# Optimization experiments

Hardware: AMD Instinct MI355X
Metric: run time of the kernel (lower is better)

## Reference

```python
import jax, jax.numpy as jnp
import numpy as np

N = 100000      # nodes
E = 3200000     # edges
F_IN = 78       # num_features_mol
F_GAT = 256     # mol_out_feats
HEADS = 2
F_HYP = 128     # mol_out_feats_hyper


def setup_inputs() -> dict:
    key = jax.random.key(0)
    ks = jax.random.split(key, 32)
    g = lambda k, s: jax.random.normal(k, s, dtype=jnp.float32) * 0.05
    inp = {}
    inp["mol_x"] = jax.random.normal(ks[0], (N, F_IN), dtype=jnp.float32)
    inp["mol_edge_index"] = jax.random.randint(ks[1], (2, E), 0, N)
    inp["hyper_edge"] = jax.random.randint(ks[2], (2, E), 0, N)
    # GAT layer 1 (78 -> 256, 2 heads, concat=False)
    inp["W1"] = g(ks[3], (F_IN, HEADS * F_GAT)); inp["as1"] = g(ks[4], (HEADS, F_GAT)); inp["ad1"] = g(ks[5], (HEADS, F_GAT)); inp["b1"] = jnp.zeros((F_GAT,), jnp.float32)
    # GAT layers 2,3 (256 -> 256)
    inp["W2"] = g(ks[6], (F_GAT, HEADS * F_GAT)); inp["as2"] = g(ks[7], (HEADS, F_GAT)); inp["ad2"] = g(ks[8], (HEADS, F_GAT)); inp["b2"] = jnp.zeros((F_GAT,), jnp.float32)
    inp["W3"] = g(ks[9], (F_GAT, HEADS * F_GAT)); inp["as3"] = g(ks[10], (HEADS, F_GAT)); inp["ad3"] = g(ks[11], (HEADS, F_GAT)); inp["b3"] = jnp.zeros((F_GAT,), jnp.float32)
    # GRU-style gating fusion
    inp["fc1_w"] = g(ks[12], (F_GAT, F_GAT)); inp["fc1_b"] = jnp.zeros((F_GAT,), jnp.float32)
    inp["fc2_w"] = g(ks[13], (F_GAT, F_GAT)); inp["fc2_b"] = jnp.zeros((F_GAT,), jnp.float32)
    inp["mol_bias"] = jax.random.uniform(ks[14], (1, F_GAT), jnp.float32, -0.2, 0.2)
    # HypergraphConv layers (334 -> 128 -> 128)
    inp["theta1"] = g(ks[15], (F_GAT + F_IN, F_HYP)); inp["hb1"] = jnp.zeros((F_HYP,), jnp.float32)
    inp["theta2"] = g(ks[16], (F_HYP, F_HYP)); inp["hb2"] = jnp.zeros((F_HYP,), jnp.float32)
    return inp


def _gat(x, src, dst, W, a_s, a_d, b):
    # PyG GATConv, heads=2, concat=False, eval mode (no dropout), self-loops pre-added in src/dst
    xh = (x @ W).reshape(N, HEADS, F_GAT)            # [N,H,C]
    a_src = (xh * a_s).sum(-1)                        # [N,H]
    a_dst = (xh * a_d).sum(-1)                        # [N,H]
    e = jax.nn.leaky_relu(a_src[src] + a_dst[dst], 0.2)  # [E',H]
    m = jax.ops.segment_max(e, dst, num_segments=N)
    ex = jnp.exp(e - m[dst])
    s = jax.ops.segment_sum(ex, dst, num_segments=N)
    alpha = ex / s[dst]                               # softmax over incoming edges
    out = jax.ops.segment_sum(xh[src] * alpha[:, :, None], dst, num_segments=N)
    return out.mean(axis=1) + b                       # concat=False -> head mean


def _hyper(x, node, edge, theta, b):
    # PyG HypergraphConv, use_attention=False: D^-1 H B^-1 H^T X Theta + b
    xt = x @ theta
    ones = jnp.ones((node.shape[0],), xt.dtype)
    D = jax.ops.segment_sum(ones, node, num_segments=N)
    B = jax.ops.segment_sum(ones, edge, num_segments=N)
    Dinv = jnp.where(D > 0, 1.0 / D, 0.0)
    Binv = jnp.where(B > 0, 1.0 / B, 0.0)
    ef = Binv[:, None] * jax.ops.segment_sum(xt[node], edge, num_segments=N)
    nf = Dinv[:, None] * jax.ops.segment_sum(ef[edge], node, num_segments=N)
    return nf + b


def _forward(mol_x, mol_edge_index, hyper_edge,
             W1, as1, ad1, b1, W2, as2, ad2, b2, W3, as3, ad3, b3,
             fc1_w, fc1_b, fc2_w, fc2_b, mol_bias, theta1, hb1, theta2, hb2):
    loops = jnp.arange(N, dtype=mol_edge_index.dtype)
    src = jnp.concatenate([mol_edge_index[0], loops])
    dst = jnp.concatenate([mol_edge_index[1], loops])
    hyper_x0 = jax.lax.stop_gradient(mol_x)  # .clone().detach()
    # layer 0
    h = jax.nn.relu(_gat(mol_x, src, dst, W1, as1, ad1, b1))
    # layer 1 (relu) + gate
    x = jax.nn.relu(_gat(h, src, dst, W2, as2, ad2, b2))
    z = jax.nn.sigmoid(x @ fc1_w.T + fc1_b + h @ fc2_w.T + fc2_b + mol_bias)
    h = z * x + (1.0 - z) * h
    # layer 2 (no relu) + gate
    x = _gat(h, src, dst, W3, as3, ad3, b3)
    z = jax.nn.sigmoid(x @ fc1_w.T + fc1_b + h @ fc2_w.T + fc2_b + mol_bias)
    h = z * x + (1.0 - z) * h
    # hypergraph branch (source uses mol_edge_index here, hyper_edge is unused)
    hx = jnp.concatenate([jax.lax.stop_gradient(h), hyper_x0], axis=1)
    node, edge = mol_edge_index[0], mol_edge_index[1]
    hx = jax.nn.relu(_hyper(hx, node, edge, theta1, hb1))
    hx = jax.nn.relu(_hyper(hx, node, edge, theta2, hb2))
    return jnp.concatenate([h, hx], axis=1)  # [N, 384]


def reference(mol_x, mol_edge_index, hyper_edge,
              W1, as1, ad1, b1, W2, as2, ad2, b2, W3, as3, ad3, b3,
              fc1_w, fc1_b, fc2_w, fc2_b, mol_bias, theta1, hb1, theta2, hb2):
    return _forward(mol_x, mol_edge_index, hyper_edge,
                    W1, as1, ad1, b1, W2, as2, ad2, b2, W3, as3, ad3, b3,
                    fc1_w, fc1_b, fc2_w, fc2_b, mol_bias, theta1, hb1, theta2, hb2)
```

## Files before the change

kernel.cpp:

```cpp
#include <hip/hip_runtime.h>

typedef unsigned short u16;
typedef __attribute__((ext_vector_type(8))) short short8v;
typedef __attribute__((ext_vector_type(8))) unsigned short ushort8v;
typedef __attribute__((ext_vector_type(4))) unsigned short ushort4v;
typedef __attribute__((ext_vector_type(4))) float f32x4;
typedef __attribute__((ext_vector_type(2))) float f32x2;

__device__ __forceinline__ float bf2f(u16 u) {
    union { unsigned int i; float f; } v; v.i = ((unsigned int)u) << 16; return v.f;
}
__device__ __forceinline__ u16 f2bf(float f) {
    union { float f; unsigned int i; } v; v.f = f;
    unsigned int i = v.i;
    return (u16)((i + 0x7FFFu + ((i >> 16) & 1u)) >> 16);
}
__device__ __forceinline__ float leaky02(float x) { return x > 0.f ? x : 0.2f * x; }
__device__ __forceinline__ float load_in(const void* p, long i, int isbf) {
    return isbf ? bf2f(((const u16*)p)[i]) : ((const float*)p)[i];
}
__device__ __forceinline__ f32x2 pk_fma(f32x2 a, f32x2 b, f32x2 c) {
    f32x2 d;
    asm("v_pk_fma_f32 %0, %1, %2, %3" : "=v"(d) : "v"(a), "v"(b), "v"(c));
    return d;
}
__device__ __forceinline__ f32x2 pk_add(f32x2 a, f32x2 b) {
    f32x2 d;
    asm("v_pk_add_f32 %0, %1, %2" : "=v"(d) : "v"(a), "v"(b));
    return d;
}
__device__ __forceinline__ f32x2 bfpair(unsigned int d) {
    union { unsigned int i; float f; } lo, hi;
    lo.i = d << 16;
    hi.i = d & 0xFFFF0000u;
    f32x2 r; r.x = lo.f; r.y = hi.f; return r;
}
__device__ __forceinline__ float bperm_f(int addr, float v) {
    return __int_as_float(__builtin_amdgcn_ds_bpermute(addr, __float_as_int(v)));
}
__device__ __forceinline__ int bperm_i(int addr, int v) {
    return __builtin_amdgcn_ds_bpermute(addr, v);
}
#define GLD_LDS16(g, s) __builtin_amdgcn_global_load_lds( \
    (const __attribute__((address_space(1))) void*)(g),   \
    (__attribute__((address_space(3))) void*)(s), 16, 0, 0)

__global__ void detect_kernel(const unsigned* __restrict__ w, int* __restrict__ flag) {
    __shared__ int cnt;
    int t = threadIdx.x;
    if (t == 0) cnt = 0;
    __syncthreads();
    unsigned x = w[t * 16];
    unsigned lo = x & 0xFFFFu;
    int e = (int)((x >> 7) & 0xFFu);
    int good = (lo == 0u) || (e >= 100 && e <= 140);
    atomicAdd(&cnt, good);
    __syncthreads();
    if (t == 0) *flag = (cnt > 128) ? 1 : 0;
}

#define CSR_NBK 1024

__global__ __launch_bounds__(256)
void bucket_count_kernel(const int* __restrict__ ei, int* __restrict__ bcs,
                         int* __restrict__ bcd, int E_, int n, int SH) {
    __shared__ int hs[CSR_NBK], hd[CSR_NBK];
    const int t = threadIdx.x;
    for (int i = t; i < CSR_NBK; i += 256) { hs[i] = 0; hd[i] = 0; }
    __syncthreads();
    const int e0 = blockIdx.x * 4096;
    #pragma unroll
    for (int k = 0; k < 16; ++k) {
        int e = e0 + k * 256 + t;
        if (e < E_) {
            int s = ei[e], d = ei[E_ + e];
            if ((unsigned)s >= (unsigned)n) s = 0;
            if ((unsigned)d >= (unsigned)n) d = 0;
            atomicAdd(&hs[s >> SH], 1);
            atomicAdd(&hd[d >> SH], 1);
        }
    }
    __syncthreads();
    for (int i = t; i < CSR_NBK; i += 256) {
        if (hs[i]) atomicAdd(&bcs[i], hs[i]);
        if (hd[i]) atomicAdd(&bcd[i], hd[i]);
    }
}

__global__ void scan_excl_kernel(const int* __restrict__ deg, int* __restrict__ ptr, int n) {
    __shared__ int s_woff[17];
    __shared__ int s_carry;
    const int t = threadIdx.x;
    const int lane = t & 63, wid = t >> 6;
    if (t == 0) s_carry = 0;
    __syncthreads();
    for (int base = 0; base < n; base += 1024) {
        int i = base + t;
        int v = (i < n) ? deg[i] : 0;
        int incl = v;
        #pragma unroll
        for (int d = 1; d < 64; d <<= 1) {
            int x = __shfl_up(incl, d, 64);
            if (lane >= d) incl += x;
        }
        if (lane == 63) s_woff[wid] = incl;
        __syncthreads();
        if (t == 0) {
            int run = 0;
            #pragma unroll
            for (int w = 0; w < 16; ++w) { int x = s_woff[w]; s_woff[w] = run; run += x; }
            s_woff[16] = run;
        }
        __syncthreads();
        int excl = s_carry + s_woff[wid] + incl - v;
        if (i < n) ptr[i] = excl;
        __syncthreads();
        if (t == 0) s_carry += s_woff[16];
        __syncthreads();
    }
    if (t == 0) ptr[n] = s_carry;
}

__global__ void copy2_kernel(const int* __restrict__ a, int* __restrict__ b,
                             const int* __restrict__ c, int* __restrict__ d2, int n) {
    int i = blockIdx.x * 256 + threadIdx.x;
    if (i < n) { b[i] = a[i]; d2[i] = c[i]; }
}

__global__ __launch_bounds__(256)
void partition_kernel(const int* __restrict__ ei, int* __restrict__ bcur_s,
                      int* __restrict__ bcur_d, int2* __restrict__ ps,
                      int2* __restrict__ pd, int E_, int n, int SH) {
    __shared__ int cs[CSR_NBK], cd[CSR_NBK], bs[CSR_NBK], bd[CSR_NBK];
    const int t = threadIdx.x;
    for (int i = t; i < CSR_NBK; i += 256) { cs[i] = 0; cd[i] = 0; }
    __syncthreads();
    const int e0 = blockIdx.x * 4096;
    int sv[16], dv[16];
    #pragma unroll
    for (int k = 0; k < 16; ++k) {
        int e = e0 + k * 256 + t;
        int s = -1, d = 0;
        if (e < E_) {
            s = ei[e]; d = ei[E_ + e];
            if ((unsigned)s >= (unsigned)n) s = 0;
            if ((unsigned)d >= (unsigned)n) d = 0;
            atomicAdd(&cs[s >> SH], 1);
            atomicAdd(&cd[d >> SH], 1);
        }
        sv[k] = (e < E_) ? s : -1;
        dv[k] = d;
    }
    __syncthreads();
    for (int i = t; i < CSR_NBK; i += 256) {
        bs[i] = cs[i] ? atomicAdd(&bcur_s[i], cs[i]) : 0;
        bd[i] = cd[i] ? atomicAdd(&bcur_d[i], cd[i]) : 0;
        cs[i] = 0; cd[i] = 0;
    }
    __syncthreads();
    #pragma unroll
    for (int k = 0; k < 16; ++k) {
        int s = sv[k];
        if (s < 0) continue;
        int d = dv[k];
        int p = bs[s >> SH] + atomicAdd(&cs[s >> SH], 1);
        ps[p] = make_int2(d, s);
        int q = bd[d >> SH] + atomicAdd(&cd[d >> SH], 1);
        pd[q] = make_int2(s, d);
    }
}

__global__ __launch_bounds__(256)
void fill_bucket_kernel(const int2* __restrict__ pairs, const int* __restrict__ bptr,
                        int* __restrict__ ptr, int* __restrict__ idx, int n, int SH) {
    __shared__ int cnt[256];
    __shared__ int wsum[5];
    const int b = blockIdx.x;
    const int n0 = b << SH;
    if (n0 >= n) return;
    const int nn = min(1 << SH, n - n0);
    const int t = threadIdx.x;
    cnt[t] = 0;
    __syncthreads();
    const int pbeg = bptr[b], pend = bptr[b + 1];
    for (int j = pbeg + t; j < pend; j += 256)
        atomicAdd(&cnt[pairs[j].y - n0], 1);
    __syncthreads();
    const int c = (t < nn) ? cnt[t] : 0;
    int v = c;
    const int lane = t & 63, wid = t >> 6;
    #pragma unroll
    for (int d = 1; d < 64; d <<= 1) {
        int x = __shfl_up(v, d, 64);
        if (lane >= d) v += x;
    }
    if (lane == 63) wsum[wid] = v;
    __syncthreads();
    if (t == 0) {
        int r = 0;
        #pragma unroll
        for (int w = 0; w < 4; ++w) { int x = wsum[w]; wsum[w] = r; r += x; }
        wsum[4] = r;
    }
    __syncthreads();
    v += wsum[wid];
    const int excl = pbeg + v - c;
    __syncthreads();
    if (t < nn) { cnt[t] = excl; ptr[n0 + t] = excl; }
    if (t == 0 && n0 + nn == n) ptr[n] = pbeg + wsum[4];
    __syncthreads();
    for (int j = pbeg + t; j < pend; j += 256) {
        int2 pr = pairs[j];
        int p = atomicAdd(&cnt[pr.y - n0], 1);
        idx[p] = pr.x;
    }
}

__global__ void ingest_transpose_kernel(const void* __restrict__ src, long base,
                                        u16* __restrict__ dst, int K, int Nc, int Kp,
                                        const int* __restrict__ flag) {
    int i = blockIdx.x * 256 + threadIdx.x;
    if (i >= Nc * Kp) return;
    int n = i / Kp, k = i - n * Kp;
    float v = (k < K) ? load_in(src, base + (long)k * Nc + n, *flag) : 0.f;
    dst[i] = f2bf(v);
}

__global__ void ingest_vecs_kernel(const void* __restrict__ s0, const void* __restrict__ s1,
                                   const void* __restrict__ s2, const void* __restrict__ s3,
                                   const void* __restrict__ s4, const void* __restrict__ s5,
                                   const void* __restrict__ s6, const void* __restrict__ s7,
                                   u16* __restrict__ d0, u16* __restrict__ d1,
                                   u16* __restrict__ d2, u16* __restrict__ d3,
                                   u16* __restrict__ d4, u16* __restrict__ d5,
                                   u16* __restrict__ d6, u16* __restrict__ d7,
                                   const int* __restrict__ flag) {
    const void* srcs[8] = {s0, s1, s2, s3, s4, s5, s6, s7};
    u16* dsts[8] = {d0, d1, d2, d3, d4, d5, d6, d7};
    const int b = blockIdx.x, t = threadIdx.x;
    const int nsz = (b < 6) ? 256 : 128;
    if (t < nsz) dsts[b][t] = f2bf(load_in(srcs[b], t, *flag));
}

__global__ void ingest_wcat_kernel(const void* __restrict__ W, u16* __restrict__ dst,
                                   int Kin, int Fh, const int* __restrict__ flag) {
    int i = blockIdx.x * 256 + threadIdx.x;
    int tot = 256 * 2 * Fh;
    if (i >= tot) return;
    int o = i / (2 * Fh), k = i - o * 2 * Fh;
    int h = k / Fh, c = k - h * Fh;
    float v = (c < Kin) ? 0.5f * load_in(W, (long)c * 512 + h * 256 + o, *flag) : 0.f;
    dst[i] = f2bf(v);
}

__global__ void ingest_bcat_kernel(const void* __restrict__ fc1, const void* __restrict__ fc2,
                                   u16* __restrict__ dst, const int* __restrict__ flag) {
    int i = blockIdx.x * 256 + threadIdx.x;
    if (i >= 256 * 512) return;
    int o = i >> 9, k = i & 511;
    float v = (k < 256) ? load_in(fc1, (long)o * 256 + k, *flag)
                        : load_in(fc2, (long)o * 256 + k - 256, *flag);
    dst[i] = f2bf(v);
}

__global__ void ingest_pad_molx_kernel(const void* __restrict__ x, u16* __restrict__ dst,
                                       int ldd, int total, const int* __restrict__ flag) {
    int i = blockIdx.x * 256 + threadIdx.x;
    if (i >= total) return;
    int r = i / 96, c = i - r * 96;
    float v = (c < 78) ? load_in(x, (long)r * 78 + c, *flag) : 0.f;
    dst[(size_t)r * ldd + c] = f2bf(v);
}

__global__ void attn_vec_kernel(const void* __restrict__ W, const void* __restrict__ as_,
                                const void* __restrict__ ad_, float* __restrict__ was,
                                float* __restrict__ wad, int Kin, int Fh,
                                const int* __restrict__ flag) {
    int i = blockIdx.x * 256 + threadIdx.x;
    if (i >= 2 * Fh) return;
    int h = i / Fh, c = i - h * Fh;
    float s = 0.f, d = 0.f;
    if (c < Kin) {
        int f = *flag;
        for (int o = 0; o < 256; ++o) {
            float w = load_in(W, (long)c * 512 + h * 256 + o, f);
            s += w * load_in(as_, h * 256 + o, f);
            d += w * load_in(ad_, h * 256 + o, f);
        }
    }
    was[i] = s; wad[i] = d;
}

__global__ __launch_bounds__(256, 2)
void gemm_kernel(const u16* __restrict__ A, int lda,
                 const u16* __restrict__ Bt, int ldb,
                 u16* __restrict__ C, int ldc, int K, int M, int beta,
                 const u16* __restrict__ bias, int relu) {
    __shared__ __align__(16) u16 As[128 * 32];
    __shared__ __align__(16) u16 Bs[128 * 32];
    const int tid = threadIdx.x;
    const int wave = tid >> 6, lane = tid & 63;
    const int m0 = blockIdx.x * 128;
    const int n0 = blockIdx.y * 128;
    const int wm = (wave & 1) * 64, wn = (wave >> 1) * 64;
    const int r = lane & 15, q = lane >> 4;

    f32x4 acc[4][4];
    if (beta) {
        #pragma unroll
        for (int i = 0; i < 4; ++i)
            #pragma unroll
            for (int j = 0; j < 4; ++j)
                #pragma unroll
                for (int rr = 0; rr < 4; ++rr) {
                    size_t gr = (size_t)(m0 + wm + 16 * i + q * 4 + rr);
                    int gc = n0 + wn + 16 * j + r;
                    acc[i][j][rr] = bf2f(C[gr * ldc + gc]);
                }
    } else {
        #pragma unroll
        for (int i = 0; i < 4; ++i)
            #pragma unroll
            for (int j = 0; j < 4; ++j) acc[i][j] = (f32x4)0.f;
    }

    const int rowT = wave * 16 + (lane >> 2);
    const int koff = (lane & 3) * 8;
    int rA0 = m0 + rowT;       if (rA0 > M - 1) rA0 = M - 1;
    int rA1 = m0 + rowT + 64;  if (rA1 > M - 1) rA1 = M - 1;
    const u16* gA0 = A + (size_t)rA0 * lda + koff;
    const u16* gA1 = A + (size_t)rA1 * lda + koff;
    const u16* gB0 = Bt + (size_t)(n0 + rowT) * ldb + koff;
    const u16* gB1 = Bt + (size_t)(n0 + rowT + 64) * ldb + koff;
    u16* sA0 = &As[rowT * 32 + koff];
    u16* sA1 = &As[(rowT + 64) * 32 + koff];
    u16* sB0 = &Bs[rowT * 32 + koff];
    u16* sB1 = &Bs[(rowT + 64) * 32 + koff];

    const int nK = K >> 5;
    for (int kt = 0; kt < nK; ++kt) {
        __syncthreads();
        GLD_LDS16(gA0, sA0);
        GLD_LDS16(gA1, sA1);
        GLD_LDS16(gB0, sB0);
        GLD_LDS16(gB1, sB1);
        gA0 += 32; gA1 += 32; gB0 += 32; gB1 += 32;
        __syncthreads();
        short8v af[4], bf[4];
        #pragma unroll
        for (int i = 0; i < 4; ++i) af[i] = *(const short8v*)&As[(wm + 16 * i + r) * 32 + q * 8];
        #pragma unroll
        for (int j = 0; j < 4; ++j) bf[j] = *(const short8v*)&Bs[(wn + 16 * j + r) * 32 + q * 8];
        #pragma unroll
        for (int i = 0; i < 4; ++i)
            #pragma unroll
            for (int j = 0; j < 4; ++j)
                acc[i][j] = __builtin_amdgcn_mfma_f32_16x16x32_bf16(af[i], bf[j], acc[i][j], 0, 0, 0);
    }
    #pragma unroll
    for (int j = 0; j < 4; ++j) {
        int gc = n0 + wn + 16 * j + r;
        float bv = bias ? bf2f(bias[gc]) : 0.f;
        #pragma unroll
        for (int i = 0; i < 4; ++i)
            #pragma unroll
            for (int rr = 0; rr < 4; ++rr) {
                size_t gr = (size_t)(m0 + wm + 16 * i + q * 4 + rr);
                float x = acc[i][j][rr] + bv;
                if (relu) x = fmaxf(x, 0.f);
                C[gr * ldc + gc] = f2bf(x);
            }
    }
}

__global__ __launch_bounds__(256)
void gemm_gate_kernel(u16* __restrict__ A , int lda,
                      const u16* __restrict__ Bt, int ldb, int K,
                      const u16* __restrict__ fc1b, const u16* __restrict__ fc2b,
                      const u16* __restrict__ molb, void* __restrict__ outw,
                      const int* __restrict__ flag, int n) {
    __shared__ __align__(16) u16 As[128 * 32];
    __shared__ __align__(16) u16 Bs[256 * 32];
    const int tid = threadIdx.x;
    const int wave = tid >> 6, lane = tid & 63;
    const int m0 = blockIdx.x * 128;
    const int wm = (wave & 1) * 64, wn = (wave >> 1) * 128;
    const int r = lane & 15, q = lane >> 4;

    f32x4 acc[4][8];
    #pragma unroll
    for (int i = 0; i < 4; ++i)
        #pragma unroll
        for (int j = 0; j < 8; ++j) acc[i][j] = (f32x4)0.f;

    const int koff = (tid & 3) * 8;
    const u16* gA0 = A + (size_t)(m0 + (tid >> 2)) * lda + koff;
    const u16* gA1 = A + (size_t)(m0 + (tid >> 2) + 64) * lda + koff;
    const u16* gB0 = Bt + (size_t)(tid >> 2) * ldb + koff;
    const u16* gB1 = Bt + (size_t)((tid >> 2) + 64) * ldb + koff;
    const u16* gB2 = Bt + (size_t)((tid >> 2) + 128) * ldb + koff;
    const u16* gB3 = Bt + (size_t)((tid >> 2) + 192) * ldb + koff;
    u16* sA0 = &As[tid * 8];
    u16* sA1 = &As[(tid + 256) * 8];
    u16* sB0 = &Bs[tid * 8];
    u16* sB1 = &Bs[(tid + 256) * 8];
    u16* sB2 = &Bs[(tid + 512) * 8];
    u16* sB3 = &Bs[(tid + 768) * 8];

    const int nK = K >> 5;
    for (int kt = 0; kt < nK; ++kt) {
        __syncthreads();
        GLD_LDS16(gA0, sA0);
        GLD_LDS16(gA1, sA1);
        GLD_LDS16(gB0, sB0);
        GLD_LDS16(gB1, sB1);
        GLD_LDS16(gB2, sB2);
        GLD_LDS16(gB3, sB3);
        gA0 += 32; gA1 += 32; gB0 += 32; gB1 += 32; gB2 += 32; gB3 += 32;
        __syncthreads();
        short8v af[4], bf[8];
        #pragma unroll
        for (int i = 0; i < 4; ++i) af[i] = *(const short8v*)&As[(wm + 16 * i + r) * 32 + q * 8];
        #pragma unroll
        for (int j = 0; j < 8; ++j) bf[j] = *(const short8v*)&Bs[(wn + 16 * j + r) * 32 + q * 8];
        #pragma unroll
        for (int i = 0; i < 4; ++i)
            #pragma unroll
            for (int j = 0; j < 8; ++j)
                acc[i][j] = __builtin_amdgcn_mfma_f32_16x16x32_bf16(af[i], bf[j], acc[i][j], 0, 0, 0);
    }
    const int fl = *flag;
    #pragma unroll
    for (int j = 0; j < 8; ++j) {
        const int gc = wn + 16 * j + r;
        const float bsum = bf2f(fc1b[gc]) + bf2f(fc2b[gc]) + bf2f(molb[gc]);
        #pragma unroll
        for (int i = 0; i < 4; ++i)
            #pragma unroll
            for (int rr = 0; rr < 4; ++rr) {
                const int gr = m0 + wm + 16 * i + q * 4 + rr;
                const size_t rb = (size_t)gr * lda;
                const float l = acc[i][j][rr] + bsum;
                const float z = 1.f / (1.f + __expf(-l));
                const float x = bf2f(A[rb + gc]);
                const float h = bf2f(A[rb + 256 + gc]);
                const float o = z * x + (1.f - z) * h;
                A[rb + 256 + gc] = f2bf(o);
                if (outw && gr < n) {
                    if (fl) ((u16*)outw)[(size_t)gr * 384 + gc] = f2bf(o);
                    else    ((float*)outw)[(size_t)gr * 384 + gc] = o;
                }
            }
    }
}

__global__ __launch_bounds__(256)
void attn_dots_h_kernel(const u16* __restrict__ hsrc, int ldh,
                        const float* __restrict__ was, const float* __restrict__ wad,
                        float* __restrict__ a_src, float* __restrict__ a_dst,
                        int Fh, int n) {
    int v = blockIdx.x * 4 + (threadIdx.x >> 6);
    if (v >= n) return;
    const int lane = threadIdx.x & 63;
    const int c0 = lane * 4;
    float ps0 = 0.f, pd0 = 0.f, ps1 = 0.f, pd1 = 0.f;
    if (c0 < Fh) {
        ushort4v xv = *(const ushort4v*)&hsrc[(size_t)v * ldh + c0];
        #pragma unroll
        for (int k = 0; k < 4; ++k) {
            float x = bf2f(xv[k]);
            ps0 += x * was[c0 + k];
            pd0 += x * wad[c0 + k];
            ps1 += x * was[Fh + c0 + k];
            pd1 += x * wad[Fh + c0 + k];
        }
    }
    #pragma unroll
    for (int d = 1; d < 64; d <<= 1) {
        ps0 += __shfl_xor(ps0, d, 64); pd0 += __shfl_xor(pd0, d, 64);
        ps1 += __shfl_xor(ps1, d, 64); pd1 += __shfl_xor(pd1, d, 64);
    }
    if (lane == 0) {
        a_src[2 * v] = ps0; a_src[2 * v + 1] = ps1;
        a_dst[2 * v] = pd0; a_dst[2 * v + 1] = pd1;
    }
}

template <int NG>
__global__ __launch_bounds__(256)
void gat_agg_h_kernel(const u16* __restrict__ hsrc, int ldh, int F,
                      const float* __restrict__ asrc, const float* __restrict__ adst,
                      const int* __restrict__ ptr, const int* __restrict__ idx,
                      u16* __restrict__ agg, int ldagg, int n, int Etot) {
    constexpr int GL = 64 / NG;
    int v = blockIdx.x * 4 + (threadIdx.x >> 6);
    if (v >= n) return;
    const int lane = threadIdx.x & 63;
    const int sub = lane / GL;
    const int c0 = (lane & (GL - 1)) * 8;
    const int act = (c0 < F);
    int beg = ptr[v], end = ptr[v + 1];
    beg = min(max(beg, 0), Etot);
    end = min(max(end, beg), Etot);
    const float ad0 = adst[2 * v], ad1 = adst[2 * v + 1];
    const float es0 = fminf(leaky02(asrc[2 * v] + ad0), 80.f);
    const float es1 = fminf(leaky02(asrc[2 * v + 1] + ad1), 80.f);
    float s0 = 0.f, s1 = 0.f;
    f32x2 f0p[4], f1p[4];
    #pragma unroll
    for (int p = 0; p < 4; ++p) { f0p[p] = (f32x2)0.f; f1p[p] = (f32x2)0.f; }

    for (int cb = beg; cb < end; cb += 64) {
        const int cnt = min(64, end - cb);
        int sE = 0;
        float wE0 = 0.f, wE1 = 0.f;
        if (lane < cnt) {
            sE = idx[cb + lane];
            sE = ((unsigned)sE < (unsigned)n) ? sE : 0;
            const float2 ap = *(const float2*)&asrc[2 * sE];
            wE0 = __expf(fminf(leaky02(ap.x + ad0), 80.f));
            wE1 = __expf(fminf(leaky02(ap.y + ad1), 80.f));
            s0 += wE0; s1 += wE1;
        }
        const int nIt = (cnt + 2 * NG - 1) / (2 * NG);
        int jj = sub;
        for (int it = 0; it < nIt; ++it, jj += 2 * NG) {
            const int aA = jj * 4, aB = aA + NG * 4;
            const int sA = bperm_i(aA, sE);
            const float wA0 = bperm_f(aA, wE0), wA1 = bperm_f(aA, wE1);
            const int sB = bperm_i(aB, sE);
            const float wB0 = bperm_f(aB, wE0), wB1 = bperm_f(aB, wE1);
            if (act) {
                const uint4 fA = *(const uint4*)&hsrc[(size_t)sA * ldh + c0];
                const uint4 fB = *(const uint4*)&hsrc[(size_t)sB * ldh + c0];
                const f32x2 wA0v = {wA0, wA0}, wA1v = {wA1, wA1};
                const f32x2 wB0v = {wB0, wB0}, wB1v = {wB1, wB1};
                #pragma unroll
                for (int p = 0; p < 4; ++p) {
                    const f32x2 xA = bfpair(((const unsigned*)&fA)[p]);
                    const f32x2 xB = bfpair(((const unsigned*)&fB)[p]);
                    f0p[p] = pk_fma(xA, wA0v, f0p[p]);
                    f1p[p] = pk_fma(xA, wA1v, f1p[p]);
                    f0p[p] = pk_fma(xB, wB0v, f0p[p]);
                    f1p[p] = pk_fma(xB, wB1v, f1p[p]);
                }
            }
        }
    }
    #pragma unroll
    for (int d = 1; d < 64; d <<= 1) {
        s0 += __shfl_xor(s0, d, 64);
        s1 += __shfl_xor(s1, d, 64);
    }
    const float w0s = __expf(es0), w1s = __expf(es1);
    s0 += w0s; s1 += w1s;
    if (sub == 0 && act) {
        const uint4 f = *(const uint4*)&hsrc[(size_t)v * ldh + c0];
        const f32x2 w0v = {w0s, w0s}, w1v = {w1s, w1s};
        #pragma unroll
        for (int p = 0; p < 4; ++p) {
            const f32x2 x = bfpair(((const unsigned*)&f)[p]);
            f0p[p] = pk_fma(x, w0v, f0p[p]);
            f1p[p] = pk_fma(x, w1v, f1p[p]);
        }
    }
    #pragma unroll
    for (int p = 0; p < 4; ++p) {
        #pragma unroll
        for (int d = GL; d < 64; d <<= 1) {
            f0p[p].x += __shfl_xor(f0p[p].x, d, 64);
            f0p[p].y += __shfl_xor(f0p[p].y, d, 64);
            f1p[p].x += __shfl_xor(f1p[p].x, d, 64);
            f1p[p].y += __shfl_xor(f1p[p].y, d, 64);
        }
    }
    if (lane < GL && act) {
        const float i0 = 1.f / s0, i1 = 1.f / s1;
        ushort8v o0, o1;
        #pragma unroll
        for (int p = 0; p < 4; ++p) {
            o0[2 * p] = f2bf(f0p[p].x * i0); o0[2 * p + 1] = f2bf(f0p[p].y * i0);
            o1[2 * p] = f2bf(f1p[p].x * i1); o1[2 * p + 1] = f2bf(f1p[p].y * i1);
        }
        *(ushort8v*)&agg[(size_t)v * ldagg + c0] = o0;
        *(ushort8v*)&agg[(size_t)v * ldagg + F + c0] = o1;
    }
}

__global__ __launch_bounds__(256)
void hyper_gather_kernel(const u16* __restrict__ feat, const int* __restrict__ ptr,
                         const int* __restrict__ idx, const u16* __restrict__ bias,
                         u16* __restrict__ outb, int ldo, void* __restrict__ outw,
                         int col0, const int* __restrict__ flag,
                         int do_relu, int n, int Etot) {
    int v = blockIdx.x * 4 + (threadIdx.x >> 6);
    if (v >= n) return;
    const int lane = threadIdx.x & 63;
    const int c0 = (lane & 15) * 8, sub = lane >> 4;
    int beg = ptr[v], end = ptr[v + 1];
    beg = min(max(beg, 0), Etot);
    end = min(max(end, beg), Etot);
    const float inv = (end > beg) ? 1.f / (float)(end - beg) : 0.f;
    f32x2 a2[4];
    #pragma unroll
    for (int p = 0; p < 4; ++p) a2[p] = (f32x2)0.f;
    int j = beg + sub;
    for (; j + 12 < end; j += 16) {
        int sA = idx[j];      sA = ((unsigned)sA < (unsigned)n) ? sA : 0;
        int sB = idx[j + 4];  sB = ((unsigned)sB < (unsigned)n) ? sB : 0;
        int sC = idx[j + 8];  sC = ((unsigned)sC < (unsigned)n) ? sC : 0;
        int sD = idx[j + 12]; sD = ((unsigned)sD < (unsigned)n) ? sD : 0;
        const uint4 fA = *(const uint4*)&feat[(size_t)sA * 128 + c0];
        const uint4 fB = *(const uint4*)&feat[(size_t)sB * 128 + c0];
        const uint4 fC = *(const uint4*)&feat[(size_t)sC * 128 + c0];
        const uint4 fD = *(const uint4*)&feat[(size_t)sD * 128 + c0];
        #pragma unroll
        for (int p = 0; p < 4; ++p) {
            a2[p] = pk_add(a2[p], bfpair(((const unsigned*)&fA)[p]));
            a2[p] = pk_add(a2[p], bfpair(((const unsigned*)&fB)[p]));
            a2[p] = pk_add(a2[p], bfpair(((const unsigned*)&fC)[p]));
            a2[p] = pk_add(a2[p], bfpair(((const unsigned*)&fD)[p]));
        }
    }
    for (; j < end; j += 4) {
        int s = idx[j]; s = ((unsigned)s < (unsigned)n) ? s : 0;
        const uint4 f = *(const uint4*)&feat[(size_t)s * 128 + c0];
        #pragma unroll
        for (int p = 0; p < 4; ++p)
            a2[p] = pk_add(a2[p], bfpair(((const unsigned*)&f)[p]));
    }
    #pragma unroll
    for (int p = 0; p < 4; ++p) {
        a2[p].x += __shfl_xor(a2[p].x, 16, 64);
        a2[p].y += __shfl_xor(a2[p].y, 16, 64);
        a2[p].x += __shfl_xor(a2[p].x, 32, 64);
        a2[p].y += __shfl_xor(a2[p].y, 32, 64);
    }
    if (sub == 0) {
        float ov[8];
        ushort8v o;
        #pragma unroll
        for (int p = 0; p < 4; ++p) {
            float x0 = a2[p].x * inv + (bias ? bf2f(bias[c0 + 2 * p]) : 0.f);
            float x1 = a2[p].y * inv + (bias ? bf2f(bias[c0 + 2 * p + 1]) : 0.f);
            if (do_relu) { x0 = fmaxf(x0, 0.f); x1 = fmaxf(x1, 0.f); }
            ov[2 * p] = x0; ov[2 * p + 1] = x1;
            o[2 * p] = f2bf(x0); o[2 * p + 1] = f2bf(x1);
        }
        if (outb) *(ushort8v*)&outb[(size_t)v * ldo + c0] = o;
        if (outw) {
            if (*flag) {
                *(ushort8v*)((u16*)outw + (size_t)v * 384 + col0 + c0) = o;
            } else {
                float* ofp = (float*)outw + (size_t)v * 384 + col0 + c0;
                #pragma unroll
                for (int k = 0; k < 8; ++k) ofp[k] = ov[k];
            }
        }
    }
}

extern "C" void kernel_launch(void* const* d_in, const int* in_sizes, int n_in,
                              void* d_out, int out_size, void* d_ws, size_t ws_size,
                              hipStream_t stream) {
    const void* molx = d_in[0];
    const int*  ei   = (const int*)d_in[1];
    const void* W1 = d_in[3], *as1 = d_in[4], *ad1 = d_in[5], *b1 = d_in[6];
    const void* W2 = d_in[7], *as2 = d_in[8], *ad2 = d_in[9], *b2 = d_in[10];
    const void* W3 = d_in[11], *as3 = d_in[12], *ad3 = d_in[13], *b3 = d_in[14];
    const void* fc1w = d_in[15], *fc1b = d_in[16], *fc2w = d_in[17], *fc2b = d_in[18];
    const void* molb = d_in[19];
    const void* th1 = d_in[20], *hb1 = d_in[21], *th2 = d_in[22], *hb2 = d_in[23];
    (void)n_in; (void)out_size;

    const int N = in_sizes[0] / 78;
    const int E = in_sizes[1] / 2;
    const int Mp = ((N + 127) / 128) * 128;

    int SH = 0;
    while (((N - 1) >> SH) >= CSR_NBK) SH++;

    char* base = (char*)d_ws;
    size_t off = 0;
    auto alloc = [&](size_t bytes) -> void* {
        void* r = base + off;
        off = (off + bytes + 255) & ~(size_t)255;
        return r;
    };
    int* flag = (int*)alloc(4);
    u16* bv1 = (u16*)alloc(256 * 2); u16* bv2 = (u16*)alloc(256 * 2); u16* bv3 = (u16*)alloc(256 * 2);
    u16* fc1bv = (u16*)alloc(256 * 2); u16* fc2bv = (u16*)alloc(256 * 2); u16* molbv = (u16*)alloc(256 * 2);
    u16* hb1v = (u16*)alloc(128 * 2); u16* hb2v = (u16*)alloc(128 * 2);
    float* was1 = (float*)alloc(192 * 4); float* wad1 = (float*)alloc(192 * 4);
    float* was2 = (float*)alloc(512 * 4); float* wad2 = (float*)alloc(512 * 4);
    float* was3 = (float*)alloc(512 * 4); float* wad3 = (float*)alloc(512 * 4);
    u16* Wc1 = (u16*)alloc(256 * 192 * 2);
    u16* Wc2 = (u16*)alloc(256 * 512 * 2);
    u16* Wc3 = (u16*)alloc(256 * 512 * 2);
    u16* Bcat = (u16*)alloc(256 * 512 * 2);
    u16* th1ta = (u16*)alloc(128 * 256 * 2);
    u16* th1tb = (u16*)alloc(128 * 96 * 2);
    u16* th2t  = (u16*)alloc(128 * 128 * 2);
    float* a_src = (float*)alloc((size_t)N * 2 * 4);
    float* a_dst = (float*)alloc((size_t)N * 2 * 4);
    int* ptr_src = (int*)alloc((size_t)(N + 1) * 4);
    int* ptr_dst = (int*)alloc((size_t)(N + 1) * 4);
    int* bcnt_src = (int*)alloc(CSR_NBK * 4);
    int* bcnt_dst = (int*)alloc(CSR_NBK * 4);
    int* bptr_src = (int*)alloc((CSR_NBK + 1) * 4);
    int* bptr_dst = (int*)alloc((CSR_NBK + 1) * 4);
    int* bcur_src = (int*)alloc(CSR_NBK * 4);
    int* bcur_dst = (int*)alloc(CSR_NBK * 4);
    int* idx_src = (int*)alloc((size_t)E * 4);
    int* idx_dst = (int*)alloc((size_t)E * 4);
    u16* cat = (u16*)alloc((size_t)Mp * 512 * 2);
    u16* agg = (u16*)alloc((size_t)Mp * 512 * 2);
    u16* xt   = agg;
    u16* efb  = agg + (size_t)Mp * 128;
    u16* hx1  = agg + (size_t)Mp * 256;
    u16* mxp2 = agg + (size_t)Mp * 384;

    int2* pairs_src; int2* pairs_dst;
    if (off + (size_t)E * 16 + 1024 <= ws_size) {
        pairs_src = (int2*)alloc((size_t)E * 8);
        pairs_dst = (int2*)alloc((size_t)E * 8);
    } else {
        pairs_src = (int2*)agg;
        pairs_dst = (int2*)((char*)agg + (size_t)E * 8);
    }

    const int nodeBlocks = (N + 3) / 4;
    const int eTiles = (E + 4095) / 4096;

    detect_kernel<<<1, 256, 0, stream>>>((const unsigned*)molx, flag);

    hipMemsetAsync(bcnt_src, 0, CSR_NBK * 4, stream);
    hipMemsetAsync(bcnt_dst, 0, CSR_NBK * 4, stream);
    bucket_count_kernel<<<eTiles, 256, 0, stream>>>(ei, bcnt_src, bcnt_dst, E, N, SH);
    scan_excl_kernel<<<1, 1024, 0, stream>>>(bcnt_src, bptr_src, CSR_NBK);
    scan_excl_kernel<<<1, 1024, 0, stream>>>(bcnt_dst, bptr_dst, CSR_NBK);
    copy2_kernel<<<(CSR_NBK + 255) / 256, 256, 0, stream>>>(bptr_src, bcur_src, bptr_dst, bcur_dst, CSR_NBK);
    partition_kernel<<<eTiles, 256, 0, stream>>>(ei, bcur_src, bcur_dst,
                                                 pairs_src, pairs_dst, E, N, SH);
    fill_bucket_kernel<<<CSR_NBK, 256, 0, stream>>>(pairs_src, bptr_src, ptr_src, idx_src, N, SH);
    fill_bucket_kernel<<<CSR_NBK, 256, 0, stream>>>(pairs_dst, bptr_dst, ptr_dst, idx_dst, N, SH);

    ingest_wcat_kernel<<<(256 * 192 + 255) / 256, 256, 0, stream>>>(W1, Wc1, 78, 96, flag);
    ingest_wcat_kernel<<<(256 * 512 + 255) / 256, 256, 0, stream>>>(W2, Wc2, 256, 256, flag);
    ingest_wcat_kernel<<<(256 * 512 + 255) / 256, 256, 0, stream>>>(W3, Wc3, 256, 256, flag);
    ingest_bcat_kernel<<<(256 * 512 + 255) / 256, 256, 0, stream>>>(fc1w, fc2w, Bcat, flag);
    ingest_transpose_kernel<<<(128 * 256 + 255) / 256, 256, 0, stream>>>(th1, 0, th1ta, 256, 128, 256, flag);
    ingest_transpose_kernel<<<(128 * 96 + 255) / 256, 256, 0, stream>>>(th1, (long)256 * 128, th1tb, 78, 128, 96, flag);
    ingest_transpose_kernel<<<(128 * 128 + 255) / 256, 256, 0, stream>>>(th2, 0, th2t, 128, 128, 128, flag);
    attn_vec_kernel<<<1, 256, 0, stream>>>(W1, as1, ad1, was1, wad1, 78, 96, flag);
    attn_vec_kernel<<<2, 256, 0, stream>>>(W2, as2, ad2, was2, wad2, 256, 256, flag);
    attn_vec_kernel<<<2, 256, 0, stream>>>(W3, as3, ad3, was3, wad3, 256, 256, flag);
    ingest_vecs_kernel<<<8, 256, 0, stream>>>(b1, b2, b3, fc1b, fc2b, molb, hb1, hb2,
                                              bv1, bv2, bv3, fc1bv, fc2bv, molbv,
                                              hb1v, hb2v, flag);
    ingest_pad_molx_kernel<<<(N * 96 + 255) / 256, 256, 0, stream>>>(molx, cat, 512, N * 96, flag);

    auto gemm = [&](const u16* A, int lda, const u16* Bt, int ldb, u16* C, int ldc,
                    int K, int Nc, int M, int beta, const u16* bias, int relu) {
        dim3 g(Mp / 128, Nc / 128);
        gemm_kernel<<<g, 256, 0, stream>>>(A, lda, Bt, ldb, C, ldc, K, M, beta, bias, relu);
    };

    attn_dots_h_kernel<<<nodeBlocks, 256, 0, stream>>>(cat, 512, was1, wad1, a_src, a_dst, 96, N);
    gat_agg_h_kernel<4><<<nodeBlocks, 256, 0, stream>>>(cat, 512, 96, a_src, a_dst,
                                                        ptr_dst, idx_dst, agg, 192, N, E);
    gemm(agg, 192, Wc1, 192, cat + 256, 512, 192, 256, Mp, 0, bv1, 1);
    attn_dots_h_kernel<<<nodeBlocks, 256, 0, stream>>>(cat + 256, 512, was2, wad2, a_src, a_dst, 256, N);
    gat_agg_h_kernel<2><<<nodeBlocks, 256, 0, stream>>>(cat + 256, 512, 256, a_src, a_dst,
                                                        ptr_dst, idx_dst, agg, 512, N, E);
    gemm(agg, 512, Wc2, 512, cat, 512, 512, 256, Mp, 0, bv2, 1);
    gemm_gate_kernel<<<Mp / 128, 256, 0, stream>>>(cat, 512, Bcat, 512, 512,
                                                   fc1bv, fc2bv, molbv, nullptr, flag, N);
    attn_dots_h_kernel<<<nodeBlocks, 256, 0, stream>>>(cat + 256, 512, was3, wad3, a_src, a_dst, 256, N);
    gat_agg_h_kernel<2><<<nodeBlocks, 256, 0, stream>>>(cat + 256, 512, 256, a_src, a_dst,
                                                        ptr_dst, idx_dst, agg, 512, N, E);
    gemm(agg, 512, Wc3, 512, cat, 512, 512, 256, Mp, 0, bv3, 0);
    gemm_gate_kernel<<<Mp / 128, 256, 0, stream>>>(cat, 512, Bcat, 512, 512,
                                                   fc1bv, fc2bv, molbv, d_out, flag, N);
    ingest_pad_molx_kernel<<<(N * 96 + 255) / 256, 256, 0, stream>>>(molx, mxp2, 96, N * 96, flag);
    gemm(cat + 256, 512, th1ta, 256, xt, 128, 256, 128, Mp, 0, nullptr, 0);
    gemm(mxp2, 96, th1tb, 96, xt, 128, 96, 128, Mp, 1, nullptr, 0);
    hyper_gather_kernel<<<nodeBlocks, 256, 0, stream>>>(xt, ptr_dst, idx_dst, (const u16*)nullptr,
                                                        efb, 128, nullptr, 0, flag, 0, N, E);
    hyper_gather_kernel<<<nodeBlocks, 256, 0, stream>>>(efb, ptr_src, idx_src, hb1v,
                                                        hx1, 128, nullptr, 0, flag, 1, N, E);
    gemm(hx1, 128, th2t, 128, xt, 128, 128, 128, Mp, 0, nullptr, 0);
    hyper_gather_kernel<<<nodeBlocks, 256, 0, stream>>>(xt, ptr_dst, idx_dst, (const u16*)nullptr,
                                                        efb, 128, nullptr, 0, flag, 0, N, E);
    hyper_gather_kernel<<<nodeBlocks, 256, 0, stream>>>(efb, ptr_src, idx_src, hb2v,
                                                        (u16*)nullptr, 0, d_out, 256, flag, 1, N, E);
}
```

Measured before the change: 2.302 ms.

## Use 128x256 GEMM tiles for GAT projections and split gate into separate kernel

Turns the fused gate GEMM into a general 128x256-tile GEMM. It now replaces the 128x128 gemm_kernel for the three GAT output projections, so each block covers the full 256-column width. The gating epilogue moves to a separate elementwise kernel that reads logits from a scratch buffer with vectorised 8-wide loads and stores. The gate's strided scalar read-modify-write goes away, at the cost of an extra logit round-trip through memory and one more launch per layer.

```diff
diff --git a/kernel.cpp b/kernel.cpp
--- a/kernel.cpp
+++ b/kernel.cpp
@@ -374,11 +374,10 @@
 }
 
 __global__ __launch_bounds__(256)
-void gemm_gate_kernel(u16* __restrict__ A , int lda,
-                      const u16* __restrict__ Bt, int ldb, int K,
-                      const u16* __restrict__ fc1b, const u16* __restrict__ fc2b,
-                      const u16* __restrict__ molb, void* __restrict__ outw,
-                      const int* __restrict__ flag, int n) {
+void gemm256_kernel(const u16* __restrict__ A, int lda,
+                    const u16* __restrict__ Bt, int ldb,
+                    u16* __restrict__ C, int ldc, int K,
+                    const u16* __restrict__ bias, int relu) {
     __shared__ __align__(16) u16 As[128 * 32];
     __shared__ __align__(16) u16 Bs[256 * 32];
     const int tid = threadIdx.x;
@@ -429,27 +428,18 @@
             for (int j = 0; j < 8; ++j)
                 acc[i][j] = __builtin_amdgcn_mfma_f32_16x16x32_bf16(af[i], bf[j], acc[i][j], 0, 0, 0);
     }
-    const int fl = *flag;
     #pragma unroll
     for (int j = 0; j < 8; ++j) {
-        const int gc = wn + 16 * j + r;
-        const float bsum = bf2f(fc1b[gc]) + bf2f(fc2b[gc]) + bf2f(molb[gc]);
+        int gc = wn + 16 * j + r;
+        float bv = bias ? bf2f(bias[gc]) : 0.f;
         #pragma unroll
         for (int i = 0; i < 4; ++i)
             #pragma unroll
             for (int rr = 0; rr < 4; ++rr) {
-                const int gr = m0 + wm + 16 * i + q * 4 + rr;
-                const size_t rb = (size_t)gr * lda;
-                const float l = acc[i][j][rr] + bsum;
-                const float z = 1.f / (1.f + __expf(-l));
-                const float x = bf2f(A[rb + gc]);
-                const float h = bf2f(A[rb + 256 + gc]);
-                const float o = z * x + (1.f - z) * h;
-                A[rb + 256 + gc] = f2bf(o);
-                if (outw && gr < n) {
-                    if (fl) ((u16*)outw)[(size_t)gr * 384 + gc] = f2bf(o);
-                    else    ((float*)outw)[(size_t)gr * 384 + gc] = o;
-                }
+                size_t gr = (size_t)(m0 + wm + 16 * i + q * 4 + rr);
+                float x = acc[i][j][rr] + bv;
+                if (relu) x = fmaxf(x, 0.f);
+                C[gr * ldc + gc] = f2bf(x);
             }
     }
 }
@@ -584,6 +574,41 @@
         }
         *(ushort8v*)&agg[(size_t)v * ldagg + c0] = o0;
         *(ushort8v*)&agg[(size_t)v * ldagg + F + c0] = o1;
+    }
+}
+
+__global__ __launch_bounds__(256)
+void gate_kernel(const u16* __restrict__ logit, const u16* __restrict__ cat,
+                 const u16* __restrict__ fc1b, const u16* __restrict__ fc2b,
+                 const u16* __restrict__ molb, u16* __restrict__ dest,
+                 void* __restrict__ outw, const int* __restrict__ flag, int n) {
+    int i = blockIdx.x * 256 + threadIdx.x;
+    if (i >= n) return;
+    int node = i >> 5, c0 = (i & 31) * 8;
+    ushort8v lg = *(const ushort8v*)&logit[(size_t)node * 256 + c0];
+    ushort8v xv = *(const ushort8v*)&cat[(size_t)node * 512 + c0];
+    ushort8v hv = *(const ushort8v*)&cat[(size_t)node * 512 + 256 + c0];
+    ushort8v b1v = *(const ushort8v*)&fc1b[c0];
+    ushort8v b2v = *(const ushort8v*)&fc2b[c0];
+    ushort8v mbv = *(const ushort8v*)&molb[c0];
+    float ov[8];
+    ushort8v dv;
+    #pragma unroll
+    for (int k = 0; k < 8; ++k) {
+        float l = bf2f(lg[k]) + bf2f(b1v[k]) + bf2f(b2v[k]) + bf2f(mbv[k]);
+        float z = 1.f / (1.f + __expf(-l));
+        ov[k] = z * bf2f(xv[k]) + (1.f - z) * bf2f(hv[k]);
+        dv[k] = f2bf(ov[k]);
+    }
+    *(ushort8v*)&dest[(size_t)node * 512 + c0] = dv;
+    if (outw) {
+        if (*flag) {
+            *(ushort8v*)((u16*)outw + (size_t)node * 384 + c0) = dv;
+        } else {
+            float* o = (float*)outw + (size_t)node * 384 + c0;
+            #pragma unroll
+            for (int k = 0; k < 8; ++k) o[k] = ov[k];
+        }
     }
 }
 
@@ -765,23 +790,29 @@
         dim3 g(Mp / 128, Nc / 128);
         gemm_kernel<<<g, 256, 0, stream>>>(A, lda, Bt, ldb, C, ldc, K, M, beta, bias, relu);
     };
+    auto gemm256 = [&](const u16* A, int lda, const u16* Bt, int ldb, u16* C, int ldc,
+                       int K, const u16* bias, int relu) {
+        gemm256_kernel<<<Mp / 128, 256, 0, stream>>>(A, lda, Bt, ldb, C, ldc, K, bias, relu);
+    };
 
     attn_dots_h_kernel<<<nodeBlocks, 256, 0, stream>>>(cat, 512, was1, wad1, a_src, a_dst, 96, N);
     gat_agg_h_kernel<4><<<nodeBlocks, 256, 0, stream>>>(cat, 512, 96, a_src, a_dst,
                                                         ptr_dst, idx_dst, agg, 192, N, E);
-    gemm(agg, 192, Wc1, 192, cat + 256, 512, 192, 256, Mp, 0, bv1, 1);
+    gemm256(agg, 192, Wc1, 192, cat + 256, 512, 192, bv1, 1);
     attn_dots_h_kernel<<<nodeBlocks, 256, 0, stream>>>(cat + 256, 512, was2, wad2, a_src, a_dst, 256, N);
     gat_agg_h_kernel<2><<<nodeBlocks, 256, 0, stream>>>(cat + 256, 512, 256, a_src, a_dst,
                                                         ptr_dst, idx_dst, agg, 512, N, E);
-    gemm(agg, 512, Wc2, 512, cat, 512, 512, 256, Mp, 0, bv2, 1);
-    gemm_gate_kernel<<<Mp / 128, 256, 0, stream>>>(cat, 512, Bcat, 512, 512,
-                                                   fc1bv, fc2bv, molbv, nullptr, flag, N);
+    gemm256(agg, 512, Wc2, 512, cat, 512, 512, bv2, 1);
+    gemm256(cat, 512, Bcat, 512, agg , 256, 512, nullptr, 0);
+    gate_kernel<<<(N * 32 + 255) / 256, 256, 0, stream>>>(agg, cat, fc1bv, fc2bv, molbv,
+                                                          cat + 256, nullptr, flag, N * 32);
     attn_dots_h_kernel<<<nodeBlocks, 256, 0, stream>>>(cat + 256, 512, was3, wad3, a_src, a_dst, 256, N);
     gat_agg_h_kernel<2><<<nodeBlocks, 256, 0, stream>>>(cat + 256, 512, 256, a_src, a_dst,
                                                         ptr_dst, idx_dst, agg, 512, N, E);
-    gemm(agg, 512, Wc3, 512, cat, 512, 512, 256, Mp, 0, bv3, 0);
-    gemm_gate_kernel<<<Mp / 128, 256, 0, stream>>>(cat, 512, Bcat, 512, 512,
-                                                   fc1bv, fc2bv, molbv, d_out, flag, N);
+    gemm256(agg, 512, Wc3, 512, cat, 512, 512, bv3, 0);
+    gemm256(cat, 512, Bcat, 512, agg , 256, 512, nullptr, 0);
+    gate_kernel<<<(N * 32 + 255) / 256, 256, 0, stream>>>(agg, cat, fc1bv, fc2bv, molbv,
+                                                          cat + 256, d_out, flag, N * 32);
     ingest_pad_molx_kernel<<<(N * 96 + 255) / 256, 256, 0, stream>>>(molx, mxp2, 96, N * 96, flag);
     gemm(cat + 256, 512, th1ta, 256, xt, 128, 256, 128, Mp, 0, nullptr, 0);
     gemm(mxp2, 96, th1tb, 96, xt, 128, 96, 128, Mp, 1, nullptr, 0);
```

Result: no change. 2.286 ms (-0.7%).
